# Performance work log

Measured on AMD Instinct MI355X. Metric: run time of the kernel, lower is better.

The kernel has to match this reference:

```python
import jax, jax.numpy as jnp
import numpy as np

N = 8192
F_IN = 1024
F_OUT = 256
ALPHA = 0.2          # LeakyReLU negative slope
ADJ_DENSITY = 0.004  # pre-symmetrization edge probability -> avg degree ~65
NEG_INF = -9.0e15    # matches -9000000000000000.0 in the torch code


def setup_inputs() -> dict:
    key = jax.random.key(0)
    k_h, k_W, k_a, k_adj = jax.random.split(key, 4)
    h = jax.random.normal(k_h, (N, F_IN), dtype=jnp.float32)
    # xavier_uniform with gain=1.414
    lim_W = 1.414 * np.sqrt(6.0 / (F_IN + F_OUT))
    W = jax.random.uniform(k_W, (F_IN, F_OUT), dtype=jnp.float32, minval=-lim_W, maxval=lim_W)
    lim_a = 1.414 * np.sqrt(6.0 / (2 * F_OUT + 1))
    a = jax.random.uniform(k_a, (2 * F_OUT, 1), dtype=jnp.float32, minval=-lim_a, maxval=lim_a)
    # sparse symmetric 0/1 adjacency (float, like the torch code's dense adj)
    u = jax.random.uniform(k_adj, (N, N))
    m = u < ADJ_DENSITY
    adj = (m | m.T).astype(jnp.float32)
    return {"h": h, "adj": adj, "W": W, "a": a}


def reference(h, adj, W, a):
    # --- GAT attention ---
    Wh = h @ W                                   # [N, F_OUT]
    Wh1 = Wh @ a[:F_OUT]                          # [N, 1]
    Wh2 = Wh @ a[F_OUT:]                          # [N, 1]
    e = jax.nn.leaky_relu(Wh1 + Wh2.T, negative_slope=ALPHA)   # [N, N]
    attention = jax.nn.softmax(jnp.where(adj > 0, e, NEG_INF), axis=1)

    # --- per-row variable-k pruning of attention + attention@attention.T ---
    n = adj.shape[0]
    diag = jnp.eye(n, dtype=bool)
    adj_nodiag = jnp.where(diag, 0.0, adj)
    s2 = jnp.count_nonzero(adj_nodiag, axis=1)    # [N] int, variable k per row

    attention2step = attention @ attention.T      # [N, N] dense GEMM
    comb = attention + attention2step
    comb = jnp.where(diag, 0.0, comb)

    # threshold = s2[i]-th largest value of row i (np.partition(row, -k)[-k])
    sorted_desc = -jnp.sort(-comb, axis=1)        # [N, N] descending per row
    idx = jnp.maximum(s2 - 1, 0)[:, None]         # clamp for s2==0 rows
    thr = jnp.take_along_axis(sorted_desc, idx, axis=1)   # [N, 1]
    # keep values >= threshold (torch code zeros values strictly < partition);
    # rows with s2 == 0 are zeroed entirely
    pruned = jnp.where((s2[:, None] > 0) & (comb >= thr), comb, 0.0)
    adj_resize = (pruned > 0).astype(jnp.float32)

    # --- output (eval mode: dropout is identity); concat=True -> ELU ---
    h_prime = attention @ Wh                      # [N, F_OUT]
    return jax.nn.elu(h_prime), adj_resize
```

## Files before the change

kernel.cpp:

```cpp
#include <hip/hip_runtime.h>
#include <cstdint>
#include <cstddef>

#define NN 8192
#define KFIN 1024
#define KFOUT 256
#define MAXD 192
#define LRALPHA 0.2f

typedef float f32x4 __attribute__((ext_vector_type(4)));

__global__ void __launch_bounds__(256) k_build_csr(
    const float* __restrict__ adj, int* __restrict__ nbr,
    int* __restrict__ deg, int* __restrict__ s2v) {
  const int wave = threadIdx.x >> 6;
  const int lane = threadIdx.x & 63;
  const int row = blockIdx.x * 4 + wave;
  const float* arow = adj + (size_t)row * NN;
  int* outp = nbr + (size_t)row * MAXD;
  int count = 0;
  int dflag = 0;
  const unsigned long long below = (1ull << lane) - 1ull;
  for (int c0 = 0; c0 < NN; c0 += 256) {
    const int c = c0 + lane * 4;
    const f32x4 v = __builtin_nontemporal_load(
        reinterpret_cast<const f32x4*>(arow + c));
    const unsigned long long m0 = __ballot(v[0] > 0.0f);
    const unsigned long long m1 = __ballot(v[1] > 0.0f);
    const unsigned long long m2 = __ballot(v[2] > 0.0f);
    const unsigned long long m3 = __ballot(v[3] > 0.0f);
    int pos = count + (int)(__popcll(m0 & below) + __popcll(m1 & below) +
                            __popcll(m2 & below) + __popcll(m3 & below));
    if (v[0] > 0.0f) { if (pos < MAXD) outp[pos] = c + 0; ++pos; if (c + 0 == row) dflag = 1; }
    if (v[1] > 0.0f) { if (pos < MAXD) outp[pos] = c + 1; ++pos; if (c + 1 == row) dflag = 1; }
    if (v[2] > 0.0f) { if (pos < MAXD) outp[pos] = c + 2; ++pos; if (c + 2 == row) dflag = 1; }
    if (v[3] > 0.0f) { if (pos < MAXD) outp[pos] = c + 3; ++pos; if (c + 3 == row) dflag = 1; }
    count += (int)(__popcll(m0) + __popcll(m1) + __popcll(m2) + __popcll(m3));
  }
  const int anyd = __any(dflag) ? 1 : 0;
  if (lane == 0) {
    deg[row] = count < MAXD ? count : MAXD;
    s2v[row] = count - anyd;
  }
}

__global__ void __launch_bounds__(256) k_gemm(
    const float* __restrict__ A, const float* __restrict__ B,
    float* __restrict__ C) {
  __shared__ float As[16][65];
  __shared__ float Bs[16][65];
  const int tid = threadIdx.x;
  const int brow = blockIdx.y * 64;
  const int bcol = blockIdx.x * 64;
  const int tx = tid & 15;
  const int ty = tid >> 4;
  float acc[4][4];
#pragma unroll
  for (int i = 0; i < 4; ++i)
#pragma unroll
    for (int j = 0; j < 4; ++j) acc[i][j] = 0.0f;
  const int ar = tid >> 2;
  const int ac = (tid & 3) << 2;
  const int br = tid >> 4;
  const int bc = (tid & 15) << 2;
  for (int k0 = 0; k0 < KFIN; k0 += 16) {
    const float4 av =
        *reinterpret_cast<const float4*>(A + (size_t)(brow + ar) * KFIN + k0 + ac);
    const float4 bv =
        *reinterpret_cast<const float4*>(B + (size_t)(k0 + br) * KFOUT + bcol + bc);
    As[ac + 0][ar] = av.x;
    As[ac + 1][ar] = av.y;
    As[ac + 2][ar] = av.z;
    As[ac + 3][ar] = av.w;
    Bs[br][bc + 0] = bv.x;
    Bs[br][bc + 1] = bv.y;
    Bs[br][bc + 2] = bv.z;
    Bs[br][bc + 3] = bv.w;
    __syncthreads();
#pragma unroll
    for (int kk = 0; kk < 16; ++kk) {
      const float a0 = As[kk][ty * 4 + 0];
      const float a1 = As[kk][ty * 4 + 1];
      const float a2 = As[kk][ty * 4 + 2];
      const float a3 = As[kk][ty * 4 + 3];
      const float b0 = Bs[kk][tx * 4 + 0];
      const float b1 = Bs[kk][tx * 4 + 1];
      const float b2 = Bs[kk][tx * 4 + 2];
      const float b3 = Bs[kk][tx * 4 + 3];
      acc[0][0] += a0 * b0; acc[0][1] += a0 * b1; acc[0][2] += a0 * b2; acc[0][3] += a0 * b3;
      acc[1][0] += a1 * b0; acc[1][1] += a1 * b1; acc[1][2] += a1 * b2; acc[1][3] += a1 * b3;
      acc[2][0] += a2 * b0; acc[2][1] += a2 * b1; acc[2][2] += a2 * b2; acc[2][3] += a2 * b3;
      acc[3][0] += a3 * b0; acc[3][1] += a3 * b1; acc[3][2] += a3 * b2; acc[3][3] += a3 * b3;
    }
    __syncthreads();
  }
#pragma unroll
  for (int i = 0; i < 4; ++i) {
#pragma unroll
    for (int j = 0; j < 4; ++j) {
      C[(size_t)(brow + ty * 4 + i) * KFOUT + bcol + tx * 4 + j] = acc[i][j];
    }
  }
}

__global__ void __launch_bounds__(256) k_rowdots(
    const float* __restrict__ Wh, const float* __restrict__ a,
    float* __restrict__ Wh1, float* __restrict__ Wh2) {
  __shared__ float sA[256];
  __shared__ float sB[256];
  const int row = blockIdx.x;
  const int t = threadIdx.x;
  const float w = Wh[(size_t)row * KFOUT + t];
  sA[t] = w * a[t];
  sB[t] = w * a[KFOUT + t];
  __syncthreads();
  for (int s = 128; s > 0; s >>= 1) {
    if (t < s) {
      sA[t] += sA[t + s];
      sB[t] += sB[t + s];
    }
    __syncthreads();
  }
  if (t == 0) {
    Wh1[row] = sA[0];
    Wh2[row] = sB[0];
  }
}

__global__ void __launch_bounds__(256) k_stats(
    const int* __restrict__ nbr, const int* __restrict__ deg,
    const float* __restrict__ Wh1, const float* __restrict__ Wh2,
    float* __restrict__ mrow, float* __restrict__ Zrow) {
  const int wave = threadIdx.x >> 6;
  const int lane = threadIdx.x & 63;
  const int row = blockIdx.x * 4 + wave;
  const int d = deg[row];
  const int* cols = nbr + (size_t)row * MAXD;
  const float w1 = Wh1[row];
  float mx = -1e30f;
  for (int t = lane; t < d; t += 64) {
    float e = w1 + Wh2[cols[t]];
    e = e > 0.0f ? e : LRALPHA * e;
    mx = fmaxf(mx, e);
  }
  for (int o = 32; o > 0; o >>= 1) mx = fmaxf(mx, __shfl_xor(mx, o));
  float sum = 0.0f;
  for (int t = lane; t < d; t += 64) {
    float e = w1 + Wh2[cols[t]];
    e = e > 0.0f ? e : LRALPHA * e;
    sum += expf(e - mx);
  }
  for (int o = 32; o > 0; o >>= 1) sum += __shfl_xor(sum, o);
  if (lane == 0) {
    mrow[row] = mx;
    Zrow[row] = (d > 0) ? sum : 1.0f;
  }
}

__global__ void __launch_bounds__(256) k_att(
    const int* __restrict__ nbr, const int* __restrict__ deg,
    const float* __restrict__ Wh1, const float* __restrict__ Wh2,
    const float* __restrict__ mrow, const float* __restrict__ Zrow,
    float* __restrict__ att, int2* __restrict__ edgesT,
    short* __restrict__ qb8) {
  const int wave = threadIdx.x >> 6;
  const int lane = threadIdx.x & 63;
  const int row = blockIdx.x * 4 + wave;
  const int d = deg[row];
  const int* cols = nbr + (size_t)row * MAXD;
  const float w1r = Wh1[row];
  const float w2r = Wh2[row];
  const float mr = mrow[row];
  const float invZr = 1.0f / Zrow[row];
  int b[7] = {0, 0, 0, 0, 0, 0, 0};
  for (int t0 = 0; t0 < d; t0 += 64) {
    const int t = t0 + lane;
    const bool act = t < d;
    const int j = act ? cols[t] : 0x7fffffff;
#pragma unroll
    for (int m = 1; m <= 7; ++m)
      b[m - 1] += (int)__popcll(__ballot(act && j < m * 1024));
    if (act) {
      float e = w1r + Wh2[j];
      e = e > 0.0f ? e : LRALPHA * e;
      att[(size_t)row * MAXD + t] = expf(e - mr) * invZr;
      float e2 = Wh1[j] + w2r;
      e2 = e2 > 0.0f ? e2 : LRALPHA * e2;
      const float v = expf(e2 - mrow[j]) / Zrow[j];
      edgesT[(size_t)row * MAXD + t] = make_int2(j, __float_as_int(v));
    }
  }
  if (lane == 0) {
    short* q = qb8 + (size_t)row * 8;
    q[0] = (short)b[0]; q[1] = (short)b[1]; q[2] = (short)b[2]; q[3] = (short)b[3];
    q[4] = (short)b[4]; q[5] = (short)b[5]; q[6] = (short)b[6]; q[7] = (short)d;
  }
}

__global__ void __launch_bounds__(512) k_twostep(
    const int* __restrict__ nbr, const int* __restrict__ deg,
    const int* __restrict__ s2v, const float* __restrict__ att,
    const int2* __restrict__ edgesT, const short* __restrict__ qb8,
    float* __restrict__ out1) {
  __shared__ float comb[NN];
  __shared__ float wvals[MAXD];
  __shared__ int kcols[MAXD];
  __shared__ short sqb[MAXD][8];
  __shared__ unsigned int hist[256];
  __shared__ unsigned int shPrefix;
  __shared__ int shRemaining;
  const int tid = threadIdx.x;
  const int wave = tid >> 6;
  const int lane = tid & 63;
  const int row = blockIdx.x;
  const f32x4 z4 = {0.0f, 0.0f, 0.0f, 0.0f};
  for (int j = tid * 4; j < NN; j += 2048)
    *reinterpret_cast<f32x4*>(&comb[j]) = z4;
  const int d = deg[row];
  const int* cols = nbr + (size_t)row * MAXD;
  const float* arow = att + (size_t)row * MAXD;
  for (int t = tid; t < d; t += 512) {
    const int c = cols[t];
    kcols[t] = c;
    wvals[t] = arow[t];
    *reinterpret_cast<int4*>(&sqb[t][0]) =
        *reinterpret_cast<const int4*>(&qb8[(size_t)c * 8]);
  }
  __syncthreads();
  {
    const int grp = lane >> 3;
    const int sub = lane & 7;
    for (int t0 = 0; t0 < d; t0 += 8) {
      const int t = t0 + grp;
      if (t < d) {
        const int qs = wave ? (int)sqb[t][wave - 1] : 0;
        const int qe = (int)sqb[t][wave];
        const float w = wvals[t];
        const int2* ek = edgesT + (size_t)kcols[t] * MAXD;
        for (int off = qs + sub; off < qe; off += 8) {
          const int2 e = ek[off];
          atomicAdd(&comb[e.x], w * __int_as_float(e.y));
        }
      }
    }
  }
  {
    const short* qr = qb8 + (size_t)row * 8;
    const int qlo = wave ? (int)qr[wave - 1] : 0;
    const int qhi = (int)qr[wave];
    for (int t = qlo + lane; t < qhi; t += 64) comb[kcols[t]] += wvals[t];
  }
  __syncthreads();
  if (tid == 0) comb[row] = 0.0f;
  __syncthreads();
  const int kk = s2v[row];
  const size_t obase = (size_t)row * NN;
  if (kk <= 0) {
    for (int j = tid * 4; j < NN; j += 2048)
      __builtin_nontemporal_store(z4, reinterpret_cast<f32x4*>(&out1[obase + j]));
    return;
  }
  unsigned int prefix = 0u;
  int remaining = kk;
  for (int pass = 0; pass < 4; ++pass) {
    const int shift = 24 - 8 * pass;
    const unsigned int pmask = (pass == 0) ? 0u : (0xFFFFFFFFu << (shift + 8));
    if (tid < 256) hist[tid] = 0u;
    __syncthreads();
    for (int j = tid * 4; j < NN; j += 2048) {
      const f32x4 cv = *reinterpret_cast<const f32x4*>(&comb[j]);
#pragma unroll
      for (int q = 0; q < 4; ++q) {
        const unsigned int u = __float_as_uint(cv[q]);
        if (u != 0u && (u & pmask) == prefix)
          atomicAdd(&hist[(u >> shift) & 255u], 1u);
      }
    }
    __syncthreads();
    if (tid < 64) {
      const int bHi = 255 - 4 * lane;
      const unsigned int c0 = hist[bHi];
      const unsigned int c1 = hist[bHi - 1];
      const unsigned int c2 = hist[bHi - 2];
      const unsigned int c3 = hist[bHi - 3];
      const unsigned int gs = c0 + c1 + c2 + c3;
      unsigned int run2 = gs;
      for (int o = 1; o < 64; o <<= 1) {
        const unsigned int tt = __shfl_up(run2, o);
        if (lane >= o) run2 += tt;
      }
      const unsigned int pre = run2 - gs;
      const unsigned int rem = (unsigned int)remaining;
      if (pre < rem && pre + gs >= rem) {
        unsigned int above;
        int digit;
        if (pre + c0 >= rem) { digit = bHi; above = pre; }
        else if (pre + c0 + c1 >= rem) { digit = bHi - 1; above = pre + c0; }
        else if (pre + c0 + c1 + c2 >= rem) { digit = bHi - 2; above = pre + c0 + c1; }
        else { digit = bHi - 3; above = pre + c0 + c1 + c2; }
        shPrefix = prefix | ((unsigned int)digit << shift);
        shRemaining = remaining - (int)above;
      }
    }
    __syncthreads();
    prefix = shPrefix;
    remaining = shRemaining;
    __syncthreads();
  }
  const float thr = __uint_as_float(prefix);
  for (int j = tid * 4; j < NN; j += 2048) {
    const f32x4 cv = *reinterpret_cast<const f32x4*>(&comb[j]);
    f32x4 ov;
    ov[0] = (cv[0] >= thr && cv[0] > 0.0f) ? 1.0f : 0.0f;
    ov[1] = (cv[1] >= thr && cv[1] > 0.0f) ? 1.0f : 0.0f;
    ov[2] = (cv[2] >= thr && cv[2] > 0.0f) ? 1.0f : 0.0f;
    ov[3] = (cv[3] >= thr && cv[3] > 0.0f) ? 1.0f : 0.0f;
    __builtin_nontemporal_store(ov, reinterpret_cast<f32x4*>(&out1[obase + j]));
  }
}

__global__ void __launch_bounds__(256) k_hprime(
    const int* __restrict__ nbr, const int* __restrict__ deg,
    const float* __restrict__ att, const float* __restrict__ Wh,
    float* __restrict__ out0) {
  __shared__ int scol[MAXD];
  __shared__ float sval[MAXD];
  const int row = blockIdx.x;
  const int c = threadIdx.x;
  const int d = deg[row];
  const int* cols = nbr + (size_t)row * MAXD;
  const float* arow = att + (size_t)row * MAXD;
  for (int t = threadIdx.x; t < d; t += 256) {
    scol[t] = cols[t];
    sval[t] = arow[t];
  }
  __syncthreads();
  float a0 = 0.0f, a1 = 0.0f, a2 = 0.0f, a3 = 0.0f;
  int t = 0;
  for (; t + 4 <= d; t += 4) {
    a0 += sval[t + 0] * Wh[(size_t)scol[t + 0] * KFOUT + c];
    a1 += sval[t + 1] * Wh[(size_t)scol[t + 1] * KFOUT + c];
    a2 += sval[t + 2] * Wh[(size_t)scol[t + 2] * KFOUT + c];
    a3 += sval[t + 3] * Wh[(size_t)scol[t + 3] * KFOUT + c];
  }
  for (; t < d; ++t) a0 += sval[t] * Wh[(size_t)scol[t] * KFOUT + c];
  const float acc = (a0 + a1) + (a2 + a3);
  out0[(size_t)row * KFOUT + c] = acc > 0.0f ? acc : expm1f(acc);
}

extern "C" void kernel_launch(void* const* d_in, const int* in_sizes, int n_in,
                              void* d_out, int out_size, void* d_ws, size_t ws_size,
                              hipStream_t stream) {
  const float* h = (const float*)d_in[0];
  const float* adj = (const float*)d_in[1];
  const float* W = (const float*)d_in[2];
  const float* a = (const float*)d_in[3];

  float* out0 = (float*)d_out;
  float* out1 = out0 + (size_t)NN * KFOUT;

  float* Wh = (float*)d_ws;
  float* Wh1 = Wh + (size_t)NN * KFOUT;
  float* Wh2 = Wh1 + NN;
  float* mrow = Wh2 + NN;
  float* Zrow = mrow + NN;
  float* att = Zrow + NN;
  float* edgesF = att + (size_t)NN * MAXD;
  int2* edgesT = (int2*)edgesF;
  int* nbr = (int*)(edgesF + (size_t)NN * MAXD * 2);
  int* deg = nbr + (size_t)NN * MAXD;
  int* s2v = deg + NN;
  short* qb8 = (short*)(s2v + NN);

  k_build_csr<<<NN / 4, 256, 0, stream>>>(adj, nbr, deg, s2v);
  dim3 ggrid(KFOUT / 64, NN / 64);
  k_gemm<<<ggrid, 256, 0, stream>>>(h, W, Wh);
  k_rowdots<<<NN, 256, 0, stream>>>(Wh, a, Wh1, Wh2);
  k_stats<<<NN / 4, 256, 0, stream>>>(nbr, deg, Wh1, Wh2, mrow, Zrow);
  k_att<<<NN / 4, 256, 0, stream>>>(nbr, deg, Wh1, Wh2, mrow, Zrow, att, edgesT, qb8);
  k_twostep<<<NN, 512, 0, stream>>>(nbr, deg, s2v, att, edgesT, qb8, out1);
  k_hprime<<<NN, 256, 0, stream>>>(nbr, deg, att, Wh, out0);
}
```

Measured before the change: 487.3 us.

## Software-pipeline two-step edge scatter with 16-lane groups and overflow pass

Rewrites the sparse two-hop accumulation so each neighbor gets 16 lanes, with 4 neighbors per wave step, instead of 8 lanes and 8 neighbors. The per-wave segment bounds are packed into 8-bit start/end pairs in shared memory, and the base offsets are precomputed. Edge loads are prefetched two steps ahead to hide global latency. Segments longer than 16 entries are finished in a separate ballot-driven pass that uses the full wave. The aim is to hide edge-load latency and improve lane utilization, at the cost of more registers and an extra loop.

```diff
diff --git a/kernel.cpp b/kernel.cpp
--- a/kernel.cpp
+++ b/kernel.cpp
@@ -205,7 +205,8 @@
   __shared__ float comb[NN];
   __shared__ float wvals[MAXD];
   __shared__ int kcols[MAXD];
-  __shared__ short sqb[MAXD][8];
+  __shared__ int kbase[MAXD];
+  __shared__ unsigned short packw[8][MAXD];
   __shared__ unsigned int hist[256];
   __shared__ unsigned int shPrefix;
   __shared__ int shRemaining;
@@ -222,25 +223,67 @@
   for (int t = tid; t < d; t += 512) {
     const int c = cols[t];
     kcols[t] = c;
+    kbase[t] = c * MAXD;
     wvals[t] = arow[t];
-    *reinterpret_cast<int4*>(&sqb[t][0]) =
-        *reinterpret_cast<const int4*>(&qb8[(size_t)c * 8]);
+    short q[8];
+    *reinterpret_cast<int4*>(q) = *reinterpret_cast<const int4*>(&qb8[(size_t)c * 8]);
+    int prev = 0;
+#pragma unroll
+    for (int w = 0; w < 8; ++w) {
+      const int qe = (int)q[w];
+      packw[w][t] = (unsigned short)(prev | (qe << 8));
+      prev = qe;
+    }
   }
   __syncthreads();
   {
-    const int grp = lane >> 3;
-    const int sub = lane & 7;
-    for (int t0 = 0; t0 < d; t0 += 8) {
-      const int t = t0 + grp;
-      if (t < d) {
-        const int qs = wave ? (int)sqb[t][wave - 1] : 0;
-        const int qe = (int)sqb[t][wave];
-        const float w = wvals[t];
-        const int2* ek = edgesT + (size_t)kcols[t] * MAXD;
-        for (int off = qs + sub; off < qe; off += 8) {
-          const int2 e = ek[off];
-          atomicAdd(&comb[e.x], w * __int_as_float(e.y));
-        }
+    const int grp = lane >> 4;
+    const int sub = lane & 15;
+    const int nsteps = (d + 3) >> 2;
+    int2 eA = make_int2(0, 0), eB = make_int2(0, 0);
+    float wA = 0.0f, wB = 0.0f;
+    bool pA_ = false, pB_ = false;
+#define PA_ISSUE(E_, W_, P_, S_)                                       \
+    {                                                                   \
+      const int t_ = (S_) * 4 + grp;                                    \
+      const bool v_ = t_ < d;                                           \
+      const unsigned pk_ = v_ ? (unsigned)packw[wave][t_] : 0u;         \
+      const int qs_ = (int)(pk_ & 255u);                                \
+      const int qe_ = (int)(pk_ >> 8);                                  \
+      P_ = v_ && (qs_ + sub) < qe_;                                     \
+      W_ = v_ ? wvals[t_] : 0.0f;                                       \
+      E_ = make_int2(0, 0);                                             \
+      if (P_) E_ = edgesT[(size_t)kbase[t_] + qs_ + sub];               \
+    }
+    if (nsteps > 0) PA_ISSUE(eA, wA, pA_, 0);
+    if (nsteps > 1) PA_ISSUE(eB, wB, pB_, 1);
+    for (int s = 0; s < nsteps; ++s) {
+      const int2 e = eA; const float w = wA; const bool p = pA_;
+      eA = eB; wA = wB; pA_ = pB_;
+      if (s + 2 < nsteps) PA_ISSUE(eB, wB, pB_, s + 2);
+      if (p) atomicAdd(&comb[e.x], w * __int_as_float(e.y));
+    }
+#undef PA_ISSUE
+  }
+  for (int t0 = 0; t0 < d; t0 += 64) {
+    const int t = t0 + lane;
+    bool big = false;
+    if (t < d) {
+      const unsigned pk = (unsigned)packw[wave][t];
+      big = ((int)(pk >> 8) - (int)(pk & 255u)) > 16;
+    }
+    unsigned long long m = __ballot(big);
+    while (m) {
+      const int tt = t0 + (int)__ffsll((long long)m) - 1;
+      m &= m - 1;
+      const unsigned pk = (unsigned)packw[wave][tt];
+      const int qs = (int)(pk & 255u);
+      const int qe = (int)(pk >> 8);
+      const float w = wvals[tt];
+      const int base = kbase[tt];
+      for (int off = qs + 16 + lane; off < qe; off += 64) {
+        const int2 e = edgesT[(size_t)base + off];
+        atomicAdd(&comb[e.x], w * __int_as_float(e.y));
       }
     }
   }
```

Result: no change. 488.6 us (+0.3%).
